# Kernel tuning notes

Hardware: AMD Instinct MI355X
Metric: run time of the kernel (lower is better)

The kernel has to match this reference:

```python
import jax, jax.numpy as jnp
import numpy as np

B, IN, H = 16384, 1024, 1024

def setup_inputs() -> dict:
    key = jax.random.key(0)
    ks = jax.random.split(key, 8)
    scale = 0.02  # keep exp-gate pre-activations in a sane range
    return {
        "x": jax.random.normal(ks[0], (B, IN), dtype=jnp.float32),
        "h": jax.random.normal(ks[1], (B, H), dtype=jnp.float32) * 0.1,
        "c": jax.random.normal(ks[2], (B, H), dtype=jnp.float32) * 0.1,
        "n": jax.random.uniform(ks[3], (B, H), dtype=jnp.float32) + 1.0,
        "m": jax.random.normal(ks[4], (B, H), dtype=jnp.float32) * 0.1,
        "Wx_w": jax.random.normal(ks[5], (4 * H, IN), dtype=jnp.float32) * scale,
        "Wh_w": jax.random.normal(ks[6], (4 * H, H), dtype=jnp.float32) * scale,
        "Wh_b": jnp.zeros((4 * H,), dtype=jnp.float32),
    }

def reference(x, h, c, n, m, Wx_w, Wh_w, Wh_b):
    # gates = Wx(x) + Wh(h)   (torch Linear: y = x @ W.T + b)
    gates = x @ Wx_w.T + h @ Wh_w.T + Wh_b  # [B, 4H]
    i_tilde, f_tilde, z, o = jnp.split(gates, 4, axis=-1)
    # exponential-gate stabilizer state
    m_new = jnp.maximum(f_tilde + m, i_tilde)
    f = jnp.exp(f_tilde + m - m_new)
    i = jnp.exp(i_tilde - m_new)
    z = jnp.tanh(z)
    o = jax.nn.sigmoid(o)
    c_new = f * c + i * z
    n_new = f * n + i
    h_new = o * (c_new / jnp.maximum(jnp.abs(n_new), 1.0))
    return (h_new, c_new, n_new, m_new)
```

## Files before the change

kernel.cpp:

```cpp
#include <hip/hip_runtime.h>
#include <cstdint>
#include <cstddef>

#define B_DIM 16384
#define H_DIM 1024
#define K_DIM 2048
#define N_DIM 4096

typedef _Float16 half8 __attribute__((ext_vector_type(8)));
typedef float floatx4 __attribute__((ext_vector_type(4)));

__device__ __forceinline__ void async_copy16(const void* g, void* l) {
  __builtin_amdgcn_global_load_lds(
      (__attribute__((address_space(1))) void*)g,
      (__attribute__((address_space(3))) void*)l,
      16, 0, 0);
}

__global__ __launch_bounds__(256) void pack_A_kernel(
    const float* __restrict__ x, const float* __restrict__ h,
    _Float16* __restrict__ A) {
  const size_t t = (size_t)blockIdx.x * 256 + threadIdx.x;
  const int row = (int)(t >> 8);
  const int col = ((int)t & 255) * 8;
  const float* src = (col < H_DIM) ? (x + (size_t)row * H_DIM + col)
                                   : (h + (size_t)row * H_DIM + (col - H_DIM));
  const float4* s4 = (const float4*)src;
  float4 v0 = s4[0];
  float4 v1 = s4[1];
  half8 r = {(_Float16)v0.x, (_Float16)v0.y, (_Float16)v0.z, (_Float16)v0.w,
             (_Float16)v1.x, (_Float16)v1.y, (_Float16)v1.z, (_Float16)v1.w};
  *(half8*)(A + t * 8) = r;
}

__global__ __launch_bounds__(256) void pack_W_kernel(
    const float* __restrict__ Wx, const float* __restrict__ Wh,
    _Float16* __restrict__ Wp) {
  const size_t t = (size_t)blockIdx.x * 256 + threadIdx.x;
  const int p = (int)(t >> 8);
  const int k = ((int)t & 255) * 8;
  const int hidx = p >> 2;
  const int g = p & 3;
  const int j = g * H_DIM + hidx;
  const float* src = (k < H_DIM) ? (Wx + (size_t)j * H_DIM + k)
                                 : (Wh + (size_t)j * H_DIM + (k - H_DIM));
  const float4* s4 = (const float4*)src;
  float4 v0 = s4[0];
  float4 v1 = s4[1];
  half8 r = {(_Float16)v0.x, (_Float16)v0.y, (_Float16)v0.z, (_Float16)v0.w,
             (_Float16)v1.x, (_Float16)v1.y, (_Float16)v1.z, (_Float16)v1.w};
  *(half8*)(Wp + (size_t)p * K_DIM + k) = r;
}

__global__ __launch_bounds__(256, 2) void slstm_gemm_fused(
    const _Float16* __restrict__ A,
    const _Float16* __restrict__ Wp,
    const float* __restrict__ c_in,
    const float* __restrict__ n_in,
    const float* __restrict__ m_in,
    const float* __restrict__ bias,
    float* __restrict__ out)
{
  __shared__ union SM {
    struct { _Float16 As[128 * 32]; _Float16 Bs[128 * 32]; } st;
    float cbuf[64 * 132];
  } sm;

  const int tid  = threadIdx.x;
  const int b0   = blockIdx.x * 128;
  const int n0   = blockIdx.y * 128;

  const int lane = tid & 63;
  const int wave = tid >> 6;
  const int wm   = wave & 1;
  const int wn   = wave >> 1;
  const int l16  = lane & 15;
  const int quad = lane >> 4;

  const _Float16* Ag0 = A  + (size_t)(b0 + (tid >> 2)) * K_DIM + (tid & 3) * 8;
  const _Float16* Ag1 = Ag0 + (size_t)64 * K_DIM;
  const _Float16* Wg0 = Wp + (size_t)(n0 + (tid >> 2)) * K_DIM + (tid & 3) * 8;
  const _Float16* Wg1 = Wg0 + (size_t)64 * K_DIM;
  _Float16* lA0 = &sm.st.As[tid * 8];
  _Float16* lA1 = &sm.st.As[(tid + 256) * 8];
  _Float16* lB0 = &sm.st.Bs[tid * 8];
  _Float16* lB1 = &sm.st.Bs[(tid + 256) * 8];

  const _Float16* aRd = &sm.st.As[(wm * 64 + l16) * 32 + quad * 8];
  const _Float16* bRd = &sm.st.Bs[(wn * 64 + l16) * 32 + quad * 8];

  floatx4 acc[4][4] = {};

  for (int kt = 0; kt < K_DIM / 32; ++kt) {
    const int ko = kt * 32;
    async_copy16(Ag0 + ko, lA0);
    async_copy16(Ag1 + ko, lA1);
    async_copy16(Wg0 + ko, lB0);
    async_copy16(Wg1 + ko, lB1);
    __syncthreads();

    half8 af[4], bf[4];
#pragma unroll
    for (int i = 0; i < 4; ++i) af[i] = *(const half8*)(aRd + i * 16 * 32);
#pragma unroll
    for (int i = 0; i < 4; ++i) bf[i] = *(const half8*)(bRd + i * 16 * 32);
#pragma unroll
    for (int mi = 0; mi < 4; ++mi)
#pragma unroll
      for (int ni = 0; ni < 4; ++ni)
        acc[mi][ni] = __builtin_amdgcn_mfma_f32_16x16x32_f16(
            af[mi], bf[ni], acc[mi][ni], 0, 0, 0);
    __syncthreads();
  }

  const size_t BH = (size_t)B_DIM * H_DIM;
  const int hh = tid & 31;
  const int rb = tid >> 5;
  const int hg = blockIdx.y * 32 + hh;
  const float bi  = bias[hg];
  const float bfv = bias[H_DIM + hg];
  const float bz  = bias[2 * H_DIM + hg];
  const float bo  = bias[3 * H_DIM + hg];

#pragma unroll
  for (int ph = 0; ph < 2; ++ph) {
    if (wm == ph) {
#pragma unroll
      for (int mi = 0; mi < 4; ++mi)
#pragma unroll
        for (int ni = 0; ni < 4; ++ni)
#pragma unroll
          for (int r = 0; r < 4; ++r)
            sm.cbuf[(mi * 16 + quad * 4 + r) * 132 + wn * 64 + ni * 16 + l16] =
                acc[mi][ni][r];
    }
    __syncthreads();

#pragma unroll
    for (int it2 = 0; it2 < 8; ++it2) {
      const int rl = it2 * 8 + rb;
      const int bg = b0 + ph * 64 + rl;
      floatx4 g = *(const floatx4*)&sm.cbuf[rl * 132 + hh * 4];
      const size_t idx = (size_t)bg * H_DIM + hg;

      const float it_ = g.x + bi;
      const float ft_ = g.y + bfv;
      float       zt_ = g.z + bz;
      const float ot_ = g.w + bo;

      const float mo = m_in[idx];
      const float fm = ft_ + mo;
      const float mn = fmaxf(fm, it_);
      const float fg = __expf(fm - mn);
      const float ig = __expf(it_ - mn);
      zt_ = fminf(fmaxf(zt_, -30.0f), 30.0f);
      const float e2 = __expf(2.0f * zt_);
      const float zg = (e2 - 1.0f) / (e2 + 1.0f);
      const float og = 1.0f / (1.0f + __expf(-ot_));
      const float cn = fg * c_in[idx] + ig * zg;
      const float nn = fg * n_in[idx] + ig;
      const float hn = og * (cn / fmaxf(fabsf(nn), 1.0f));

      out[idx]          = hn;
      out[BH + idx]     = cn;
      out[2 * BH + idx] = nn;
      out[3 * BH + idx] = mn;
    }
    __syncthreads();
  }
}

extern "C" void kernel_launch(void* const* d_in, const int* in_sizes, int n_in,
                              void* d_out, int out_size, void* d_ws, size_t ws_size,
                              hipStream_t stream) {
  (void)in_sizes; (void)n_in; (void)out_size; (void)ws_size;
  const float* x   = (const float*)d_in[0];
  const float* h   = (const float*)d_in[1];
  const float* c   = (const float*)d_in[2];
  const float* n   = (const float*)d_in[3];
  const float* m   = (const float*)d_in[4];
  const float* Wxw = (const float*)d_in[5];
  const float* Whw = (const float*)d_in[6];
  const float* Whb = (const float*)d_in[7];

  _Float16* A  = (_Float16*)d_ws;
  _Float16* Wp = (_Float16*)((char*)d_ws + (size_t)B_DIM * K_DIM * sizeof(_Float16));

  pack_A_kernel<<<(B_DIM * (K_DIM / 8)) / 256, 256, 0, stream>>>(x, h, A);
  pack_W_kernel<<<(N_DIM * (K_DIM / 8)) / 256, 256, 0, stream>>>(Wxw, Whw, Wp);

  dim3 grid(B_DIM / 128, N_DIM / 128);
  slstm_gemm_fused<<<grid, 256, 0, stream>>>(A, Wp, c, n, m, Whb, (float*)d_out);
}
```

Measured before the change: 853.8 us.

## Rewrite GEMM with 256x256 tiles, double-buffered async LDS pipeline and swizzling

```diff
diff --git a/kernel.cpp b/kernel.cpp
--- a/kernel.cpp
+++ b/kernel.cpp
@@ -52,7 +52,7 @@
   *(half8*)(Wp + (size_t)p * K_DIM + k) = r;
 }
 
-__global__ __launch_bounds__(256, 2) void slstm_gemm_fused(
+__global__ __launch_bounds__(512, 2) void slstm_gemm_fused(
     const _Float16* __restrict__ A,
     const _Float16* __restrict__ Wp,
     const float* __restrict__ c_in,
@@ -62,91 +62,137 @@
     float* __restrict__ out)
 {
   __shared__ union SM {
-    struct { _Float16 As[128 * 32]; _Float16 Bs[128 * 32]; } st;
-    float cbuf[64 * 132];
+    struct { _Float16 a[2][2][256 * 32]; _Float16 b[2][2][256 * 32]; } g;
+    float cbuf[64 * 268];
   } sm;
-
-  const int tid  = threadIdx.x;
-  const int b0   = blockIdx.x * 128;
-  const int n0   = blockIdx.y * 128;
+  char* const lds = (char*)&sm;
+
+  const int tid = threadIdx.x;
+
+  const int swz = ((int)blockIdx.x & 7) * 128 + ((int)blockIdx.x >> 3);
+  const int b0 = (swz >> 4) * 256;
+  const int n0 = (swz & 15) * 256;
 
   const int lane = tid & 63;
   const int wave = tid >> 6;
-  const int wm   = wave & 1;
-  const int wn   = wave >> 1;
+  const int wm   = wave >> 2;
+  const int wn   = wave & 3;
   const int l16  = lane & 15;
   const int quad = lane >> 4;
 
-  const _Float16* Ag0 = A  + (size_t)(b0 + (tid >> 2)) * K_DIM + (tid & 3) * 8;
-  const _Float16* Ag1 = Ag0 + (size_t)64 * K_DIM;
-  const _Float16* Wg0 = Wp + (size_t)(n0 + (tid >> 2)) * K_DIM + (tid & 3) * 8;
-  const _Float16* Wg1 = Wg0 + (size_t)64 * K_DIM;
-  _Float16* lA0 = &sm.st.As[tid * 8];
-  _Float16* lA1 = &sm.st.As[(tid + 256) * 8];
-  _Float16* lB0 = &sm.st.Bs[tid * 8];
-  _Float16* lB1 = &sm.st.Bs[(tid + 256) * 8];
-
-  const _Float16* aRd = &sm.st.As[(wm * 64 + l16) * 32 + quad * 8];
-  const _Float16* bRd = &sm.st.Bs[(wn * 64 + l16) * 32 + quad * 8];
-
-  floatx4 acc[4][4] = {};
-
-  for (int kt = 0; kt < K_DIM / 32; ++kt) {
-    const int ko = kt * 32;
-    async_copy16(Ag0 + ko, lA0);
-    async_copy16(Ag1 + ko, lA1);
-    async_copy16(Wg0 + ko, lB0);
-    async_copy16(Wg1 + ko, lB1);
-    __syncthreads();
-
-    half8 af[4], bf[4];
-#pragma unroll
-    for (int i = 0; i < 4; ++i) af[i] = *(const half8*)(aRd + i * 16 * 32);
-#pragma unroll
-    for (int i = 0; i < 4; ++i) bf[i] = *(const half8*)(bRd + i * 16 * 32);
-#pragma unroll
-    for (int mi = 0; mi < 4; ++mi)
-#pragma unroll
-      for (int ni = 0; ni < 4; ++ni)
-        acc[mi][ni] = __builtin_amdgcn_mfma_f32_16x16x32_f16(
-            af[mi], bf[ni], acc[mi][ni], 0, 0, 0);
-    __syncthreads();
+  const int srow = tid >> 2;
+  const int gch  = (tid & 3) ^ ((tid >> 3) & 3);
+  const _Float16* const Ag = A  + (size_t)(b0 + srow) * K_DIM + gch * 8;
+  const _Float16* const Bg = Wp + (size_t)(n0 + srow) * K_DIM + gch * 8;
+
+  const int rsw = (quad ^ ((l16 >> 1) & 3)) * 8;
+
+  floatx4 acc[8][4] = {};
+
+#define LDS_A(buf, tk) (lds + (size_t)((((buf) * 2 + (tk)) * 16384)) + 16 * tid)
+#define LDS_B(buf, tk) (lds + 65536 + (size_t)((((buf) * 2 + (tk)) * 16384)) + 16 * tid)
+#define STAGE_A(buf, tk, kt) do {                        \
+    const _Float16* g_ = Ag + (kt) * 32;                 \
+    char* l_ = LDS_A(buf, tk);                           \
+    async_copy16(g_, l_);                                \
+    async_copy16(g_ + (size_t)128 * K_DIM, l_ + 8192);   \
+  } while (0)
+#define STAGE_B(buf, tk, kt) do {                        \
+    const _Float16* g_ = Bg + (kt) * 32;                 \
+    char* l_ = LDS_B(buf, tk);                           \
+    async_copy16(g_, l_);                                \
+    async_copy16(g_ + (size_t)128 * K_DIM, l_ + 8192);   \
+  } while (0)
+#define KBARRIER() asm volatile("s_barrier" ::: "memory")
+
+  STAGE_A(0, 0, 0);
+  STAGE_B(0, 0, 0);
+  STAGE_A(0, 1, 1);
+  STAGE_B(0, 1, 1);
+  asm volatile("s_waitcnt vmcnt(4)" ::: "memory");
+  KBARRIER();
+
+#pragma unroll 2
+  for (int it = 0; it < 32; ++it) {
+    const int cur = it & 1;
+    const int nxt = cur ^ 1;
+    const int ks  = it * 2 + 2;
+    const bool notlast = (it < 31);
+#pragma unroll
+    for (int p = 0; p < 4; ++p) {
+      const int tk = p >> 1;
+      const int mh = p & 1;
+      const _Float16* As_ =
+          (const _Float16*)(lds + (size_t)((cur * 2 + tk) * 16384));
+      const _Float16* Bs_ =
+          (const _Float16*)(lds + 65536 + (size_t)((cur * 2 + tk) * 16384));
+      half8 af[4], bf[4];
+#pragma unroll
+      for (int a = 0; a < 4; ++a)
+        af[a] = *(const half8*)(As_ + (wm * 128 + mh * 64 + a * 16 + l16) * 32 + rsw);
+#pragma unroll
+      for (int b = 0; b < 4; ++b)
+        bf[b] = *(const half8*)(Bs_ + (wn * 64 + b * 16 + l16) * 32 + rsw);
+      if (notlast) {
+        if      (p == 0) STAGE_A(nxt, 0, ks);
+        else if (p == 1) STAGE_B(nxt, 0, ks);
+        else if (p == 2) STAGE_A(nxt, 1, ks + 1);
+        else             STAGE_B(nxt, 1, ks + 1);
+      }
+      KBARRIER();
+      __builtin_amdgcn_s_setprio(1);
+#pragma unroll
+      for (int a = 0; a < 4; ++a)
+#pragma unroll
+        for (int b = 0; b < 4; ++b)
+          acc[mh * 4 + a][b] = __builtin_amdgcn_mfma_f32_16x16x32_f16(
+              af[a], bf[b], acc[mh * 4 + a][b], 0, 0, 0);
+      __builtin_amdgcn_s_setprio(0);
+      if (p == 1) {
+        if (notlast) asm volatile("s_waitcnt vmcnt(4)" ::: "memory");
+        else         asm volatile("s_waitcnt vmcnt(0)" ::: "memory");
+      } else if (p == 3) {
+        if (notlast) asm volatile("s_waitcnt vmcnt(4)" ::: "memory");
+      }
+      KBARRIER();
+    }
   }
 
   const size_t BH = (size_t)B_DIM * H_DIM;
-  const int hh = tid & 31;
-  const int rb = tid >> 5;
-  const int hg = blockIdx.y * 32 + hh;
+  const int hh = tid & 63;
+  const int rb = tid >> 6;
+  const int hg = (n0 >> 2) + hh;
   const float bi  = bias[hg];
   const float bfv = bias[H_DIM + hg];
   const float bz  = bias[2 * H_DIM + hg];
   const float bo  = bias[3 * H_DIM + hg];
 
 #pragma unroll
-  for (int ph = 0; ph < 2; ++ph) {
-    if (wm == ph) {
-#pragma unroll
-      for (int mi = 0; mi < 4; ++mi)
-#pragma unroll
-        for (int ni = 0; ni < 4; ++ni)
+  for (int ph = 0; ph < 4; ++ph) {
+    if (wm == (ph >> 1)) {
+      const int fb = (ph & 1) * 4;
+#pragma unroll
+      for (int a = 0; a < 4; ++a)
+#pragma unroll
+        for (int j = 0; j < 4; ++j)
 #pragma unroll
           for (int r = 0; r < 4; ++r)
-            sm.cbuf[(mi * 16 + quad * 4 + r) * 132 + wn * 64 + ni * 16 + l16] =
-                acc[mi][ni][r];
+            sm.cbuf[(a * 16 + quad * 4 + r) * 268 + wn * 64 + j * 16 + l16] =
+                acc[fb + a][j][r];
     }
     __syncthreads();
 
 #pragma unroll
-    for (int it2 = 0; it2 < 8; ++it2) {
-      const int rl = it2 * 8 + rb;
+    for (int itr = 0; itr < 8; ++itr) {
+      const int rl = itr * 8 + rb;
       const int bg = b0 + ph * 64 + rl;
-      floatx4 g = *(const floatx4*)&sm.cbuf[rl * 132 + hh * 4];
+      floatx4 gv = *(const floatx4*)&sm.cbuf[rl * 268 + hh * 4];
       const size_t idx = (size_t)bg * H_DIM + hg;
 
-      const float it_ = g.x + bi;
-      const float ft_ = g.y + bfv;
-      float       zt_ = g.z + bz;
-      const float ot_ = g.w + bo;
+      const float it_ = gv.x + bi;
+      const float ft_ = gv.y + bfv;
+      float       zt_ = gv.z + bz;
+      const float ot_ = gv.w + bo;
 
       const float mo = m_in[idx];
       const float fm = ft_ + mo;
@@ -189,6 +235,5 @@
   pack_A_kernel<<<(B_DIM * (K_DIM / 8)) / 256, 256, 0, stream>>>(x, h, A);
   pack_W_kernel<<<(N_DIM * (K_DIM / 8)) / 256, 256, 0, stream>>>(Wxw, Whw, Wp);
 
-  dim3 grid(B_DIM / 128, N_DIM / 128);
-  slstm_gemm_fused<<<grid, 256, 0, stream>>>(A, Wp, c, n, m, Whb, (float*)d_out);
-}
+  slstm_gemm_fused<<<1024, 512, 0, stream>>>(A, Wp, c, n, m, Whb, (float*)d_out);
+}
```

Measured after the change: 789.0 us. 1.08x faster.
